# Performance work log

Measured on AMD Instinct MI355X. Metric: run time of the kernel, lower is better.

The kernel has to match this reference:

```python
import jax, jax.numpy as jnp
import numpy as np

N, E, G = 139264, 278528, 8192   # nodes, edges, graphs
H, DIN, DOUT, C = 256, 2, 3, 60
EPS = 1e-5


def setup_inputs() -> dict:
    key = jax.random.key(0)
    ks = jax.random.split(key, 24)
    inp = {
        "node_features": jax.random.normal(ks[0], (N, DIN), jnp.float32),
        "src": jax.random.randint(ks[1], (E,), 0, N, jnp.int32),
        "dst": jax.random.randint(ks[2], (E,), 0, N, jnp.int32),
        "node2graph": jnp.sort(jax.random.randint(ks[3], (N,), 0, G, jnp.int32)),
        "W_emb": jax.random.normal(ks[4], (DIN, H), jnp.float32) * 0.5,
        "b_emb": jnp.zeros((H,), jnp.float32),
        "W_conv1": jax.random.normal(ks[5], (H, H), jnp.float32) / np.sqrt(H),
        "b_conv1": jnp.zeros((H,), jnp.float32),
        "W_conv2": jax.random.normal(ks[6], (H, H), jnp.float32) / np.sqrt(H),
        "b_conv2": jnp.zeros((H,), jnp.float32),
        # 6 BatchNorm layers (2 in block_1, 2 in block_2, 2 in block_3), eval mode
        "bn_gamma": jnp.ones((6, H), jnp.float32),
        "bn_beta": jnp.zeros((6, H), jnp.float32),
        "bn_mean": jax.random.normal(ks[7], (6, H), jnp.float32) * 0.1,
        "bn_var": jax.random.uniform(ks[8], (6, H), jnp.float32, 0.5, 1.5),
        "W_out": jax.random.normal(ks[9], (H, DOUT), jnp.float32) / np.sqrt(H),
        "b_out": jnp.zeros((DOUT,), jnp.float32),
        "W_ci": jax.random.normal(ks[10], (DOUT, H), jnp.float32) * 0.5,
        "b_ci": jnp.zeros((H,), jnp.float32),
        "W_b3a": jax.random.normal(ks[11], (H, H), jnp.float32) / np.sqrt(H),
        "b_b3a": jnp.zeros((H,), jnp.float32),
        "W_b3b": jax.random.normal(ks[12], (H, H), jnp.float32) / np.sqrt(H),
        "b_b3b": jnp.zeros((H,), jnp.float32),
        "W_cls": jax.random.normal(ks[13], (H, C), jnp.float32) / np.sqrt(H),
        "b_cls": jnp.zeros((C,), jnp.float32),
    }
    return inp


def reference(node_features, src, dst, node2graph,
              W_emb, b_emb, W_conv1, b_conv1, W_conv2, b_conv2,
              bn_gamma, bn_beta, bn_mean, bn_var,
              W_out, b_out, W_ci, b_ci,
              W_b3a, b_b3a, W_b3b, b_b3b, W_cls, b_cls):
    ones_e = jnp.ones((E,), jnp.float32)
    deg_out = jnp.clip(jax.ops.segment_sum(ones_e, src, N), 1.0)  # out-degree
    deg_in = jnp.clip(jax.ops.segment_sum(ones_e, dst, N), 1.0)   # in-degree
    n_out = jax.lax.rsqrt(deg_out)[:, None]
    n_in = jax.lax.rsqrt(deg_in)[:, None]

    def graph_conv(x, W, b):  # DGL GraphConv, norm='both'
        m = (x * n_out)[src]                               # [E,H] gather
        agg = jax.ops.segment_sum(m, dst, N)               # [N,H] scatter-add
        return (agg * n_in) @ W + b

    def bn(x, i):  # eval-mode BatchNorm1d
        inv = jax.lax.rsqrt(bn_var[i] + EPS)
        return (x - bn_mean[i]) * (bn_gamma[i] * inv) + bn_beta[i]

    # embedding
    x = node_features @ W_emb + b_emb                      # [N,H]
    # conv block 1 (dropout is identity in eval)
    h = graph_conv(x, W_conv1, b_conv1)
    h = x + jax.nn.relu(bn(jax.nn.relu(bn(h, 0)), 1))
    x = h
    # conv block 2
    h = graph_conv(h, W_conv2, b_conv2)
    h = x + jax.nn.relu(bn(jax.nn.relu(bn(h, 2)), 3))
    # 3D pose head
    h3d = h @ W_out + b_out                                # [N,3]
    # per-graph mean (dgl.mean_nodes)
    gsum = jax.ops.segment_sum(h3d, node2graph, G)         # [G,3]
    gcnt = jnp.clip(jax.ops.segment_sum(jnp.ones((N,), jnp.float32), node2graph, G), 1.0)
    gmean = gsum / gcnt[:, None]
    # classification head
    z = gmean @ W_ci + b_ci
    z = jax.nn.relu(bn(z @ W_b3a + b_b3a, 4))
    z = jax.nn.relu(bn(z @ W_b3b + b_b3b, 5))
    label = z @ W_cls + b_cls                              # [G,60]
    return (h3d, label)
```

## Files before the change

### kernel.cpp

```cpp
#include <hip/hip_runtime.h>


#define NN 139264
#define EE 278528
#define GG 8192
#define NBLK 544
#define EBLK 1088

typedef float f32x4 __attribute__((ext_vector_type(4)));
typedef __bf16 bf16x8 __attribute__((ext_vector_type(8)));
typedef unsigned short u16x8 __attribute__((ext_vector_type(8)));
typedef unsigned short u16x4 __attribute__((ext_vector_type(4)));

__device__ __forceinline__ float bf2f(unsigned short u) {
    unsigned int i = ((unsigned int)u) << 16;
    float f;
    __builtin_memcpy(&f, &i, 4);
    return f;
}
__device__ __forceinline__ unsigned short f2bf(float f) {
    unsigned int i;
    __builtin_memcpy(&i, &f, 4);
    i += 0x7fffu + ((i >> 16) & 1u);
    return (unsigned short)(i >> 16);
}
__device__ __forceinline__ unsigned short bfbits(float f) {
    __bf16 b = (__bf16)f;
    return __builtin_bit_cast(unsigned short, b);
}

#define OFF_DEG_OUT ((size_t)0)
#define OFF_DEG_IN  ((size_t)557056)
#define ZERO_BYTES  ((size_t)1114112)
#define OFF_T       ((size_t)1114112)
#define OFF_NOUT    ((size_t)2785280)
#define OFF_NIN     ((size_t)3342336)
#define OFF_ROWPTR  ((size_t)3899392)
#define OFF_CURSOR  ((size_t)4460544)
#define OFF_CSRS    ((size_t)5017600)
#define OFF_WT2     ((size_t)6131712)
#define OFF_WTA     ((size_t)6262784)
#define OFF_WTB     ((size_t)6393856)
#define OFF_WTCLS   ((size_t)6524928)
#define OFF_WOT     ((size_t)6557696)
#define OFF_BNS     ((size_t)6565888)
#define OFF_BNH     ((size_t)6572032)
#define OFF_TAB     ((size_t)6578176)
#define OFF_PP      ((size_t)6587392)
#define OFF_BSUM    ((size_t)6595584)
#define OFF_R3      ((size_t)6599680)
#define OFF_H1W     ((size_t)8270848)


__global__ void k_deg(const int* __restrict__ src, const int* __restrict__ dst,
                      int* __restrict__ deg_out, int* __restrict__ deg_in) {
    int e = blockIdx.x * 256 + threadIdx.x;
    if (e < EE) {
        atomicAdd(&deg_out[src[e]], 1);
        atomicAdd(&deg_in[dst[e]], 1);
    }
}

__global__ void k_scan1(const int* __restrict__ deg, int* __restrict__ part, int* __restrict__ bsum) {
    __shared__ int sh[256];
    int t = threadIdx.x, gid = blockIdx.x * 256 + t;
    int v = deg[gid];
    sh[t] = v;
    __syncthreads();
#pragma unroll
    for (int off = 1; off < 256; off <<= 1) {
        int a = (t >= off) ? sh[t - off] : 0;
        __syncthreads();
        sh[t] += a;
        __syncthreads();
    }
    part[gid] = sh[t] - v;
    if (t == 255) bsum[blockIdx.x] = sh[t];
}

__global__ void k_scan2(int* __restrict__ bsum) {
    __shared__ int sh[1024];
    int t = threadIdx.x;
    int v = (t < NBLK) ? bsum[t] : 0;
    sh[t] = v;
    __syncthreads();
#pragma unroll
    for (int off = 1; off < 1024; off <<= 1) {
        int a = (t >= off) ? sh[t - off] : 0;
        __syncthreads();
        sh[t] += a;
        __syncthreads();
    }
    if (t < NBLK) bsum[t] = sh[t] - v;
}

__global__ void k_scan3(int* __restrict__ rp, const int* __restrict__ bsum, int* __restrict__ cursor,
                        const int* __restrict__ dego, const int* __restrict__ degi,
                        float* __restrict__ n_out, float* __restrict__ n_in) {
    int t = threadIdx.x, gid = blockIdx.x * 256 + t;
    int v = rp[gid] + bsum[blockIdx.x];
    rp[gid] = v;
    cursor[gid] = v;
    if (gid == 0) rp[NN] = EE;
    n_out[gid] = rsqrtf((float)max(dego[gid], 1));
    n_in[gid]  = rsqrtf((float)max(degi[gid], 1));
}

__global__ void k_fill(const int* __restrict__ src, const int* __restrict__ dst,
                       int* __restrict__ cursor, int* __restrict__ csr) {
    int e = blockIdx.x * 256 + threadIdx.x;
    int d = dst[e];
    int pos = atomicAdd(&cursor[d], 1);
    csr[pos] = src[e];
}

__global__ void k_rowstats(const int* __restrict__ rp, const int* __restrict__ csr,
                           const float* __restrict__ n_out, const float* __restrict__ n_in,
                           const float* __restrict__ nf, float* __restrict__ T) {
    int r = blockIdx.x * 256 + threadIdx.x;
    int e0 = rp[r], e1 = rp[r + 1];
    float S0 = 0.f, S1 = 0.f, S2 = 0.f;
    for (int e = e0; e < e1; e++) {
        int s = csr[e];
        float sc = n_out[s];
        S0 = fmaf(sc, nf[2 * s], S0);
        S1 = fmaf(sc, nf[2 * s + 1], S1);
        S2 += sc;
    }
    float ni = n_in[r];
    T[3 * r]     = S0 * ni;
    T[3 * r + 1] = S1 * ni;
    T[3 * r + 2] = S2 * ni;
}

__global__ void k_prep(const float* __restrict__ Wc2, const float* __restrict__ Wb3a,
                       const float* __restrict__ Wb3b,
                       unsigned short* __restrict__ wt2, unsigned short* __restrict__ wta,
                       unsigned short* __restrict__ wtb,
                       const float* __restrict__ wcls, unsigned short* __restrict__ tcls,
                       const float* __restrict__ g, const float* __restrict__ b,
                       const float* __restrict__ m, const float* __restrict__ v,
                       float* __restrict__ bns, float* __restrict__ bnh,
                       const float* __restrict__ Wout, unsigned short* __restrict__ wot,
                       const float* __restrict__ Wemb, const float* __restrict__ bemb,
                       const float* __restrict__ Wc1, const float* __restrict__ bc1,
                       const float* __restrict__ bc2,
                       float* __restrict__ TAB, float* __restrict__ PP) {
    int t = blockIdx.x * 256 + threadIdx.x;
    int y = blockIdx.y;
    if (y < 3) {
        int k = t >> 8, n = t & 255;
        const float* w = (y == 0) ? Wc2 : (y == 1) ? Wb3a : Wb3b;
        unsigned short* o = (y == 0) ? wt2 : (y == 1) ? wta : wtb;
        o[n * 256 + k] = f2bf(w[t]);
    } else if (y == 3) {
        if (t < 16384) {
            int n = t >> 8, k = t & 255;
            tcls[t] = (n < 60) ? f2bf(wcls[k * 60 + n]) : (unsigned short)0;
        }
    } else if (y == 4) {
        if (t < 1536) {
            float inv = rsqrtf(v[t] + 1e-5f);
            float s = g[t] * inv;
            bns[t] = s;
            bnh[t] = b[t] - m[t] * s;
        }
    } else if (y == 5) {
        if (t < 4096) {
            int n = t >> 8, k = t & 255;
            wot[t] = (n < 3) ? f2bf(Wout[k * 3 + n]) : (unsigned short)0;
        }
    } else if (y == 6) {
        if (t < 256) {
            int c = t;
            float inv0 = rsqrtf(v[c] + 1e-5f);
            float s0 = g[c] * inv0;
            float h0 = b[c] - m[c] * s0;
            float e0 = 0.f, e1 = 0.f, e2 = 0.f;
            for (int k = 0; k < 256; k++) {
                float w = Wc1[k * 256 + c];
                e0 = fmaf(Wemb[k], w, e0);
                e1 = fmaf(Wemb[256 + k], w, e1);
                e2 = fmaf(bemb[k], w, e2);
            }
            TAB[c]        = e0 * s0;
            TAB[256 + c]  = e1 * s0;
            TAB[512 + c]  = e2 * s0;
            TAB[768 + c]  = fmaf(bc1[c], s0, h0);
            float inv1 = rsqrtf(v[256 + c] + 1e-5f);
            float s1 = g[256 + c] * inv1;
            TAB[1024 + c] = s1;
            TAB[1280 + c] = b[256 + c] - m[256 + c] * s1;
            TAB[1536 + c] = Wemb[c];
            TAB[1792 + c] = Wemb[256 + c];
            TAB[2048 + c] = bemb[c];
        }
    } else {
        if (t < 256) {
            int cp = t;
            int w = cp >> 6, rs = (cp >> 2) & 15, nt = cp & 3;
            int c = w * 64 + nt * 16 + rs;
            PP[cp] = bc2[c];
            float inv2 = rsqrtf(v[512 + c] + 1e-5f);
            float s2 = g[512 + c] * inv2;
            PP[256 + cp] = s2;
            PP[512 + cp] = b[512 + c] - m[512 + c] * s2;
            float inv3 = rsqrtf(v[768 + c] + 1e-5f);
            float s3 = g[768 + c] * inv3;
            PP[768 + cp] = s3;
            PP[1024 + cp] = b[768 + c] - m[768 + c] * s3;
            PP[1280 + cp] = Wout[c * 3];
            PP[1536 + cp] = Wout[c * 3 + 1];
            PP[1792 + cp] = Wout[c * 3 + 2];
        }
    }
}

__launch_bounds__(256)
__global__ void k_conv1(const float* __restrict__ T, const float* __restrict__ nf,
                        const float* __restrict__ TAB, const float* __restrict__ n_out,
                        const unsigned short* __restrict__ Wt2, const unsigned short* __restrict__ wot,
                        unsigned short* __restrict__ h1w, float* __restrict__ R3) {
    __shared__ unsigned char tileY[64 * 512];
    int lane = threadIdx.x & 63, wave = threadIdx.x >> 6;
    int wrow = blockIdx.x * 64;
    int rsel = lane & 15, kq = lane >> 4;

    {
        int wu = __builtin_amdgcn_readfirstlane(wave);
        const float* tb = TAB + wu * 64;
        int row = wrow + lane;
        float t0 = T[3 * row], t1 = T[3 * row + 1], t2 = T[3 * row + 2];
        float2 p = *(const float2*)(nf + 2 * (size_t)row);
        float f0 = p.x, f1 = p.y;
        float no = n_out[row];
        int sw = (lane & 7) << 4;
        unsigned char* wb = tileY + lane * 512;
#pragma unroll
        for (int jj = 0; jj < 8; jj++) {
            int co = jj * 8;
            f32x4 ew0a = *(const f32x4*)(tb + co),        ew0b = *(const f32x4*)(tb + co + 4);
            f32x4 ew1a = *(const f32x4*)(tb + 256 + co),  ew1b = *(const f32x4*)(tb + 256 + co + 4);
            f32x4 ew2a = *(const f32x4*)(tb + 512 + co),  ew2b = *(const f32x4*)(tb + 512 + co + 4);
            f32x4 c0a  = *(const f32x4*)(tb + 768 + co),  c0b  = *(const f32x4*)(tb + 768 + co + 4);
            f32x4 s1a  = *(const f32x4*)(tb + 1024 + co), s1b  = *(const f32x4*)(tb + 1024 + co + 4);
            f32x4 h1a  = *(const f32x4*)(tb + 1280 + co), h1b  = *(const f32x4*)(tb + 1280 + co + 4);
            f32x4 w0a  = *(const f32x4*)(tb + 1536 + co), w0b  = *(const f32x4*)(tb + 1536 + co + 4);
            f32x4 w1a  = *(const f32x4*)(tb + 1792 + co), w1b  = *(const f32x4*)(tb + 1792 + co + 4);
            f32x4 bea  = *(const f32x4*)(tb + 2048 + co), beb  = *(const f32x4*)(tb + 2048 + co + 4);
            u16x8 o;
#pragma unroll
            for (int j = 0; j < 4; j++) {
                float z = fmaf(t0, ew0a[j], fmaf(t1, ew1a[j], fmaf(t2, ew2a[j], c0a[j])));
                z = fmaxf(z, 0.f);
                z = fmaxf(fmaf(z, s1a[j], h1a[j]), 0.f);
                float yv = z + fmaf(f0, w0a[j], fmaf(f1, w1a[j], bea[j]));
                o[j] = bfbits(yv * no);
            }
#pragma unroll
            for (int j = 0; j < 4; j++) {
                float z = fmaf(t0, ew0b[j], fmaf(t1, ew1b[j], fmaf(t2, ew2b[j], c0b[j])));
                z = fmaxf(z, 0.f);
                z = fmaxf(fmaf(z, s1b[j], h1b[j]), 0.f);
                float yv = z + fmaf(f0, w0b[j], fmaf(f1, w1b[j], beb[j]));
                o[4 + j] = bfbits(yv * no);
            }
            int cbyte = (wu * 64 + co) * 2;
            *(u16x8*)(wb + (cbyte ^ sw)) = o;
        }
    }
    __syncthreads();

    bool w0w = (wave == 0);
    f32x4 acc[4][4];
    f32x4 acc3[4];
    f32x4 zero = {0.f, 0.f, 0.f, 0.f};
#pragma unroll
    for (int i = 0; i < 4; i++) {
        acc3[i] = zero;
#pragma unroll
        for (int j = 0; j < 4; j++) acc[i][j] = zero;
    }
#pragma unroll
    for (int kt = 0; kt < 8; kt++) {
        int cb = kt * 64 + kq * 16;
        int k0 = kt * 32 + kq * 8;
        bf16x8 afr[4];
#pragma unroll
        for (int mt = 0; mt < 4; mt++) {
            int ar = mt * 16 + rsel;
            u16x8 au = *(const u16x8*)(tileY + ar * 512 + (cb ^ ((ar & 7) << 4)));
            afr[mt] = __builtin_bit_cast(bf16x8, au);
        }
        bf16x8 bfr[4];
#pragma unroll
        for (int nt = 0; nt < 4; nt++) {
            u16x8 bu = *(const u16x8*)(Wt2 + (size_t)(wave * 64 + nt * 16 + rsel) * 256 + k0);
            bfr[nt] = __builtin_bit_cast(bf16x8, bu);
        }
        bf16x8 bw;
        if (w0w) {
            u16x8 bu = *(const u16x8*)(wot + (size_t)rsel * 256 + k0);
            bw = __builtin_bit_cast(bf16x8, bu);
        }
#pragma unroll
        for (int mt = 0; mt < 4; mt++) {
#pragma unroll
            for (int nt = 0; nt < 4; nt++)
                acc[mt][nt] = __builtin_amdgcn_mfma_f32_16x16x32_bf16(afr[mt], bfr[nt], acc[mt][nt], 0, 0, 0);
            if (w0w)
                acc3[mt] = __builtin_amdgcn_mfma_f32_16x16x32_bf16(afr[mt], bw, acc3[mt], 0, 0, 0);
        }
    }

#pragma unroll
    for (int mt = 0; mt < 4; mt++) {
#pragma unroll
        for (int r = 0; r < 4; r++) {
            int row = wrow + mt * 16 + kq * 4 + r;
            u16x4 o;
#pragma unroll
            for (int nt = 0; nt < 4; nt++) o[nt] = bfbits(acc[mt][nt][r]);
            *(u16x4*)(h1w + (size_t)row * 256 + wave * 64 + rsel * 4) = o;
        }
    }

    if (w0w && rsel < 3) {
#pragma unroll
        for (int mt = 0; mt < 4; mt++)
#pragma unroll
            for (int r = 0; r < 4; r++) {
                int row = wrow + mt * 16 + kq * 4 + r;
                R3[(size_t)row * 3 + rsel] = acc3[mt][r] / n_out[row];
            }
    }
}

__launch_bounds__(256)
__global__ void k_gconv(const int* __restrict__ rp, const int* __restrict__ csr,
                        const float* __restrict__ n_in, const unsigned short* __restrict__ h1w,
                        const float* __restrict__ PP, const float* __restrict__ bout,
                        const float* __restrict__ R3, float* __restrict__ h3d) {
    int hw = threadIdx.x >> 5;
    int l = threadIdx.x & 31;
    int c0 = l * 8;

    float bc[8], s0[8], h0[8], s1[8], h1v[8], w0[8], w1[8], w2[8];
#pragma unroll
    for (int j = 0; j < 8; j += 4) {
        *(float4*)(bc + j)  = *(const float4*)(PP + c0 + j);
        *(float4*)(s0 + j)  = *(const float4*)(PP + 256 + c0 + j);
        *(float4*)(h0 + j)  = *(const float4*)(PP + 512 + c0 + j);
        *(float4*)(s1 + j)  = *(const float4*)(PP + 768 + c0 + j);
        *(float4*)(h1v + j) = *(const float4*)(PP + 1024 + c0 + j);
        *(float4*)(w0 + j)  = *(const float4*)(PP + 1280 + c0 + j);
        *(float4*)(w1 + j)  = *(const float4*)(PP + 1536 + c0 + j);
        *(float4*)(w2 + j)  = *(const float4*)(PP + 1792 + c0 + j);
    }
    float b0 = bout[0], b1 = bout[1], b2v = bout[2];

    int rbase = blockIdx.x * 64 + hw * 8;
#pragma unroll 1
    for (int i = 0; i < 8; i++) {
        int row = rbase + i;
        int e0 = rp[row], e1 = rp[row + 1];
        float a[8] = {0.f, 0.f, 0.f, 0.f, 0.f, 0.f, 0.f, 0.f};
        for (int e = e0; e < e1; e++) {
            int s = csr[e];
            u16x8 v = *(const u16x8*)(h1w + ((size_t)s << 8) + c0);
#pragma unroll
            for (int j = 0; j < 8; j++) a[j] += bf2f(v[j]);
        }
        float ni = n_in[row];
        float p0 = 0.f, p1 = 0.f, p2 = 0.f;
#pragma unroll
        for (int j = 0; j < 8; j++) {
            float y = fmaf(a[j], ni, bc[j]);
            y = fmaxf(fmaf(y, s0[j], h0[j]), 0.f);
            y = fmaxf(fmaf(y, s1[j], h1v[j]), 0.f);
            p0 = fmaf(y, w0[j], p0);
            p1 = fmaf(y, w1[j], p1);
            p2 = fmaf(y, w2[j], p2);
        }
#pragma unroll
        for (int m = 1; m < 32; m <<= 1) {
            p0 += __shfl_xor(p0, m, 32);
            p1 += __shfl_xor(p1, m, 32);
            p2 += __shfl_xor(p2, m, 32);
        }
        if (l == 0) {
            size_t o = (size_t)row * 3;
            h3d[o]     = p0 + R3[o]     + b0;
            h3d[o + 1] = p1 + R3[o + 1] + b1;
            h3d[o + 2] = p2 + R3[o + 2] + b2v;
        }
    }
}

__launch_bounds__(64)
__global__ void k_head(const int* __restrict__ n2g, const float* __restrict__ h3d,
                       const float* __restrict__ Wci, const float* __restrict__ bci,
                       const unsigned short* __restrict__ wta, const float* __restrict__ ba,
                       const unsigned short* __restrict__ wtb, const float* __restrict__ bb,
                       const unsigned short* __restrict__ wtcls, const float* __restrict__ bcls,
                       const float* __restrict__ bns, const float* __restrict__ bnh,
                       float* __restrict__ label) {
    __shared__ unsigned char tileA[8192];
    __shared__ unsigned char tileB[8192];
    int lane = threadIdx.x;
    int wrow = blockIdx.x * 16;
    int rsel = lane & 15, kq = lane >> 4;
    int g = wrow + rsel;

    int lo = 0, hi = NN;
    while (lo < hi) { int mid = (lo + hi) >> 1; if (n2g[mid] < g) lo = mid + 1; else hi = mid; }
    int s = lo;
    hi = NN;
    while (lo < hi) { int mid = (lo + hi) >> 1; if (n2g[mid] < g + 1) lo = mid + 1; else hi = mid; }
    int e = lo;
    float m0 = 0.f, m1 = 0.f, m2 = 0.f;
    for (int j = s; j < e; j++) {
        m0 += h3d[(size_t)j * 3];
        m1 += h3d[(size_t)j * 3 + 1];
        m2 += h3d[(size_t)j * 3 + 2];
    }
    float inv = 1.f / fmaxf((float)(e - s), 1.f);
    m0 *= inv; m1 *= inv; m2 *= inv;

    f32x4 zero = {0.f, 0.f, 0.f, 0.f};
    f32x4 acc[16];
#pragma unroll
    for (int i = 0; i < 16; i++) acc[i] = zero;

#pragma unroll
    for (int kt = 0; kt < 8; kt++) {
        int k0 = kt * 32 + kq * 8;
        u16x8 au;
#pragma unroll
        for (int j = 0; j < 8; j++)
            au[j] = f2bf(fmaf(m0, Wci[k0 + j], fmaf(m1, Wci[256 + k0 + j],
                         fmaf(m2, Wci[512 + k0 + j], bci[k0 + j]))));
        bf16x8 af = __builtin_bit_cast(bf16x8, au);
#pragma unroll
        for (int nt = 0; nt < 16; nt++) {
            u16x8 bu = *(const u16x8*)(wta + (size_t)(nt * 16 + rsel) * 256 + k0);
            acc[nt] = __builtin_amdgcn_mfma_f32_16x16x32_bf16(af, __builtin_bit_cast(bf16x8, bu), acc[nt], 0, 0, 0);
        }
    }
#pragma unroll
    for (int nt = 0; nt < 16; nt++) {
        int col = nt * 16 + rsel;
        float bcv = ba[col];
        float sc = bns[4 * 256 + col], h = bnh[4 * 256 + col];
#pragma unroll
        for (int r = 0; r < 4; r++) {
            float y = fmaxf(fmaf(acc[nt][r] + bcv, sc, h), 0.f);
            int rr = kq * 4 + r;
            *(unsigned short*)(tileA + rr * 512 + ((col * 2) ^ ((rr & 7) << 4))) = f2bf(y);
        }
    }

#pragma unroll
    for (int i = 0; i < 16; i++) acc[i] = zero;
#pragma unroll
    for (int kt = 0; kt < 8; kt++) {
        int cb = kt * 64 + kq * 16;
        u16x8 au = *(const u16x8*)(tileA + rsel * 512 + (cb ^ ((rsel & 7) << 4)));
        bf16x8 af = __builtin_bit_cast(bf16x8, au);
        int k0 = kt * 32 + kq * 8;
#pragma unroll
        for (int nt = 0; nt < 16; nt++) {
            u16x8 bu = *(const u16x8*)(wtb + (size_t)(nt * 16 + rsel) * 256 + k0);
            acc[nt] = __builtin_amdgcn_mfma_f32_16x16x32_bf16(af, __builtin_bit_cast(bf16x8, bu), acc[nt], 0, 0, 0);
        }
    }
#pragma unroll
    for (int nt = 0; nt < 16; nt++) {
        int col = nt * 16 + rsel;
        float bcv = bb[col];
        float sc = bns[5 * 256 + col], h = bnh[5 * 256 + col];
#pragma unroll
        for (int r = 0; r < 4; r++) {
            float y = fmaxf(fmaf(acc[nt][r] + bcv, sc, h), 0.f);
            int rr = kq * 4 + r;
            *(unsigned short*)(tileB + rr * 512 + ((col * 2) ^ ((rr & 7) << 4))) = f2bf(y);
        }
    }

    f32x4 acc3[4];
#pragma unroll
    for (int i = 0; i < 4; i++) acc3[i] = zero;
#pragma unroll
    for (int kt = 0; kt < 8; kt++) {
        int cb = kt * 64 + kq * 16;
        u16x8 au = *(const u16x8*)(tileB + rsel * 512 + (cb ^ ((rsel & 7) << 4)));
        bf16x8 af = __builtin_bit_cast(bf16x8, au);
        int k0 = kt * 32 + kq * 8;
#pragma unroll
        for (int nt = 0; nt < 4; nt++) {
            u16x8 bu = *(const u16x8*)(wtcls + (size_t)(nt * 16 + rsel) * 256 + k0);
            acc3[nt] = __builtin_amdgcn_mfma_f32_16x16x32_bf16(af, __builtin_bit_cast(bf16x8, bu), acc3[nt], 0, 0, 0);
        }
    }
    int rowb = wrow + kq * 4;
#pragma unroll
    for (int nt = 0; nt < 4; nt++) {
        int col = nt * 16 + rsel;
        if (col < 60) {
            float bcv = bcls[col];
#pragma unroll
            for (int r = 0; r < 4; r++)
                label[(size_t)(rowb + r) * 60 + col] = acc3[nt][r] + bcv;
        }
    }
}

extern "C" void kernel_launch(void* const* d_in, const int* in_sizes, int n_in,
                              void* d_out, int out_size, void* d_ws, size_t ws_size,
                              hipStream_t stream) {
    const float* nf   = (const float*)d_in[0];
    const int* src    = (const int*)d_in[1];
    const int* dst    = (const int*)d_in[2];
    const int* n2g    = (const int*)d_in[3];
    const float* Wemb = (const float*)d_in[4];
    const float* bemb = (const float*)d_in[5];
    const float* Wc1  = (const float*)d_in[6];
    const float* bc1  = (const float*)d_in[7];
    const float* Wc2  = (const float*)d_in[8];
    const float* bc2  = (const float*)d_in[9];
    const float* bng  = (const float*)d_in[10];
    const float* bnb  = (const float*)d_in[11];
    const float* bnm  = (const float*)d_in[12];
    const float* bnv  = (const float*)d_in[13];
    const float* Wout = (const float*)d_in[14];
    const float* bout = (const float*)d_in[15];
    const float* Wci  = (const float*)d_in[16];
    const float* bci  = (const float*)d_in[17];
    const float* Wb3a = (const float*)d_in[18];
    const float* bb3a = (const float*)d_in[19];
    const float* Wb3b = (const float*)d_in[20];
    const float* bb3b = (const float*)d_in[21];
    const float* Wcls = (const float*)d_in[22];
    const float* bcls = (const float*)d_in[23];

    char* ws = (char*)d_ws;
    int* deg_out = (int*)(ws + OFF_DEG_OUT);
    int* deg_in  = (int*)(ws + OFF_DEG_IN);
    float* T     = (float*)(ws + OFF_T);
    float* n_out = (float*)(ws + OFF_NOUT);
    float* n_inp = (float*)(ws + OFF_NIN);
    int* row_ptr = (int*)(ws + OFF_ROWPTR);
    int* cursor  = (int*)(ws + OFF_CURSOR);
    int* csr_src = (int*)(ws + OFF_CSRS);
    int* bsum    = (int*)(ws + OFF_BSUM);
    unsigned short* wt2   = (unsigned short*)(ws + OFF_WT2);
    unsigned short* wta   = (unsigned short*)(ws + OFF_WTA);
    unsigned short* wtb   = (unsigned short*)(ws + OFF_WTB);
    unsigned short* wtcls = (unsigned short*)(ws + OFF_WTCLS);
    unsigned short* wot   = (unsigned short*)(ws + OFF_WOT);
    float* bns = (float*)(ws + OFF_BNS);
    float* bnh = (float*)(ws + OFF_BNH);
    float* TAB = (float*)(ws + OFF_TAB);
    float* PP  = (float*)(ws + OFF_PP);
    float* R3  = (float*)(ws + OFF_R3);
    unsigned short* h1w = (unsigned short*)(ws + OFF_H1W);

    float* h3d_out   = (float*)d_out;
    float* label_out = (float*)d_out + (size_t)NN * 3;

    hipMemsetAsync(ws, 0, ZERO_BYTES, stream);

    k_deg<<<EBLK, 256, 0, stream>>>(src, dst, deg_out, deg_in);
    k_scan1<<<NBLK, 256, 0, stream>>>(deg_in, row_ptr, bsum);
    k_scan2<<<1, 1024, 0, stream>>>(bsum);
    k_scan3<<<NBLK, 256, 0, stream>>>(row_ptr, bsum, cursor, deg_out, deg_in, n_out, n_inp);
    k_fill<<<EBLK, 256, 0, stream>>>(src, dst, cursor, csr_src);
    k_prep<<<dim3(256, 8), 256, 0, stream>>>(Wc2, Wb3a, Wb3b, wt2, wta, wtb,
                                             Wcls, wtcls, bng, bnb, bnm, bnv, bns, bnh,
                                             Wout, wot, Wemb, bemb, Wc1, bc1, bc2, TAB, PP);
    k_rowstats<<<NBLK, 256, 0, stream>>>(row_ptr, csr_src, n_out, n_inp, nf, T);

    k_conv1<<<NN / 64, 256, 0, stream>>>(T, nf, TAB, n_out, wt2, wot, h1w, R3);
    k_gconv<<<NN / 64, 256, 0, stream>>>(row_ptr, csr_src, n_inp, h1w, PP, bout, R3, h3d_out);
    k_head<<<GG / 16, 64, 0, stream>>>(n2g, h3d_out, Wci, bci, wta, bb3a, wtb, bb3b,
                                       wtcls, bcls, bns, bnh, label_out);
}
```

Baseline: 230.1 us.

## Merge graph preprocessing kernels into one cooperative kernel with grid syncs

Replaces the memset plus seven preprocessing launches (degree count, three-stage scan, CSR fill, weight prep, row stats) with a single cooperative kernel that separates the phases with grid.sync(). The block-sum scan now runs in one block using three elements per thread. The goal is to remove launch gaps and per-kernel ramp-up between these small stages. In exchange it adds several grid-wide barriers, and it needs all 544 blocks to be co-resident; if they are not, the cooperative launch can fail.

```diff
diff --git a/kernel.cpp b/kernel.cpp
--- a/kernel.cpp
+++ b/kernel.cpp
@@ -1,11 +1,13 @@
 #include <hip/hip_runtime.h>
-
+#include <hip/hip_cooperative_groups.h>
+
+
+namespace cg = cooperative_groups;
 
 #define NN 139264
 #define EE 278528
 #define GG 8192
 #define NBLK 544
-#define EBLK 1088
 
 typedef float f32x4 __attribute__((ext_vector_type(4)));
 typedef __bf16 bf16x8 __attribute__((ext_vector_type(8)));
@@ -31,7 +33,6 @@
 
 #define OFF_DEG_OUT ((size_t)0)
 #define OFF_DEG_IN  ((size_t)557056)
-#define ZERO_BYTES  ((size_t)1114112)
 #define OFF_T       ((size_t)1114112)
 #define OFF_NOUT    ((size_t)2785280)
 #define OFF_NIN     ((size_t)3342336)
@@ -51,168 +52,176 @@
 #define OFF_R3      ((size_t)6599680)
 #define OFF_H1W     ((size_t)8270848)
 
-
-__global__ void k_deg(const int* __restrict__ src, const int* __restrict__ dst,
-                      int* __restrict__ deg_out, int* __restrict__ deg_in) {
-    int e = blockIdx.x * 256 + threadIdx.x;
-    if (e < EE) {
+__launch_bounds__(256)
+__global__ void k_gprep(const int* __restrict__ src, const int* __restrict__ dst,
+                        const float* __restrict__ nf,
+                        int* __restrict__ deg_out, int* __restrict__ deg_in,
+                        int* __restrict__ rp, int* __restrict__ cursor, int* __restrict__ csr,
+                        float* __restrict__ n_out, float* __restrict__ n_in,
+                        int* __restrict__ bsum, float* __restrict__ T,
+                        const float* __restrict__ Wc2, const float* __restrict__ Wb3a,
+                        const float* __restrict__ Wb3b,
+                        unsigned short* __restrict__ wt2, unsigned short* __restrict__ wta,
+                        unsigned short* __restrict__ wtb,
+                        const float* __restrict__ wcls, unsigned short* __restrict__ tcls,
+                        const float* __restrict__ bng, const float* __restrict__ bnb,
+                        const float* __restrict__ bnm, const float* __restrict__ bnv,
+                        float* __restrict__ bns, float* __restrict__ bnh,
+                        const float* __restrict__ Wout, unsigned short* __restrict__ wot,
+                        const float* __restrict__ Wemb, const float* __restrict__ bemb,
+                        const float* __restrict__ Wc1, const float* __restrict__ bc1,
+                        const float* __restrict__ bc2,
+                        float* __restrict__ TAB, float* __restrict__ PP) {
+    cg::grid_group grid = cg::this_grid();
+    __shared__ int sh[256];
+    __shared__ int shS[NBLK];
+    __shared__ int shT[256];
+    int tid = threadIdx.x;
+    int gtid = blockIdx.x * 256 + tid;
+
+    deg_out[gtid] = 0;
+    deg_in[gtid] = 0;
+    if (gtid < 65536) {
+        int k = gtid >> 8, n = gtid & 255;
+        wt2[n * 256 + k] = f2bf(Wc2[gtid]);
+        wta[n * 256 + k] = f2bf(Wb3a[gtid]);
+        wtb[n * 256 + k] = f2bf(Wb3b[gtid]);
+    }
+    if (gtid < 16384) {
+        int n = gtid >> 8, k = gtid & 255;
+        tcls[gtid] = (n < 60) ? f2bf(wcls[k * 60 + n]) : (unsigned short)0;
+    }
+    if (gtid < 1536) {
+        float inv = rsqrtf(bnv[gtid] + 1e-5f);
+        float s = bng[gtid] * inv;
+        bns[gtid] = s;
+        bnh[gtid] = bnb[gtid] - bnm[gtid] * s;
+    }
+    if (gtid < 4096) {
+        int n = gtid >> 8, k = gtid & 255;
+        wot[gtid] = (n < 3) ? f2bf(Wout[k * 3 + n]) : (unsigned short)0;
+    }
+    if (gtid >= 131072 && gtid < 131328) {
+        int c = gtid - 131072;
+        float inv0 = rsqrtf(bnv[c] + 1e-5f);
+        float s0 = bng[c] * inv0;
+        float h0 = bnb[c] - bnm[c] * s0;
+        float e0 = 0.f, e1 = 0.f, e2 = 0.f;
+        for (int k = 0; k < 256; k++) {
+            float w = Wc1[k * 256 + c];
+            e0 = fmaf(Wemb[k], w, e0);
+            e1 = fmaf(Wemb[256 + k], w, e1);
+            e2 = fmaf(bemb[k], w, e2);
+        }
+        TAB[c]        = e0 * s0;
+        TAB[256 + c]  = e1 * s0;
+        TAB[512 + c]  = e2 * s0;
+        TAB[768 + c]  = fmaf(bc1[c], s0, h0);
+        float inv1 = rsqrtf(bnv[256 + c] + 1e-5f);
+        float s1 = bng[256 + c] * inv1;
+        TAB[1024 + c] = s1;
+        TAB[1280 + c] = bnb[256 + c] - bnm[256 + c] * s1;
+        TAB[1536 + c] = Wemb[c];
+        TAB[1792 + c] = Wemb[256 + c];
+        TAB[2048 + c] = bemb[c];
+    }
+    if (gtid >= 131328 && gtid < 131584) {
+        int cp = gtid - 131328;
+        int w = cp >> 6, rs = (cp >> 2) & 15, nt = cp & 3;
+        int c = w * 64 + nt * 16 + rs;
+        PP[cp] = bc2[c];
+        float inv2 = rsqrtf(bnv[512 + c] + 1e-5f);
+        float s2 = bng[512 + c] * inv2;
+        PP[256 + cp] = s2;
+        PP[512 + cp] = bnb[512 + c] - bnm[512 + c] * s2;
+        float inv3 = rsqrtf(bnv[768 + c] + 1e-5f);
+        float s3 = bng[768 + c] * inv3;
+        PP[768 + cp] = s3;
+        PP[1024 + cp] = bnb[768 + c] - bnm[768 + c] * s3;
+        PP[1280 + cp] = Wout[c * 3];
+        PP[1536 + cp] = Wout[c * 3 + 1];
+        PP[1792 + cp] = Wout[c * 3 + 2];
+    }
+    grid.sync();
+
+    for (int e = gtid; e < EE; e += NN) {
         atomicAdd(&deg_out[src[e]], 1);
         atomicAdd(&deg_in[dst[e]], 1);
     }
-}
-
-__global__ void k_scan1(const int* __restrict__ deg, int* __restrict__ part, int* __restrict__ bsum) {
-    __shared__ int sh[256];
-    int t = threadIdx.x, gid = blockIdx.x * 256 + t;
-    int v = deg[gid];
-    sh[t] = v;
-    __syncthreads();
-#pragma unroll
-    for (int off = 1; off < 256; off <<= 1) {
-        int a = (t >= off) ? sh[t - off] : 0;
+    grid.sync();
+
+    {
+        int v = deg_in[gtid];
+        sh[tid] = v;
         __syncthreads();
-        sh[t] += a;
+#pragma unroll
+        for (int off = 1; off < 256; off <<= 1) {
+            int a = (tid >= off) ? sh[tid - off] : 0;
+            __syncthreads();
+            sh[tid] += a;
+            __syncthreads();
+        }
+        rp[gtid] = sh[tid] - v;
+        if (tid == 255) bsum[blockIdx.x] = sh[tid];
+    }
+    grid.sync();
+
+    if (blockIdx.x == 0) {
+        for (int i = tid; i < NBLK; i += 256) shS[i] = bsum[i];
         __syncthreads();
-    }
-    part[gid] = sh[t] - v;
-    if (t == 255) bsum[blockIdx.x] = sh[t];
-}
-
-__global__ void k_scan2(int* __restrict__ bsum) {
-    __shared__ int sh[1024];
-    int t = threadIdx.x;
-    int v = (t < NBLK) ? bsum[t] : 0;
-    sh[t] = v;
-    __syncthreads();
-#pragma unroll
-    for (int off = 1; off < 1024; off <<= 1) {
-        int a = (t >= off) ? sh[t - off] : 0;
+        int i0 = 3 * tid;
+        int a0 = (i0 < NBLK) ? shS[i0] : 0;
+        int a1 = (i0 + 1 < NBLK) ? shS[i0 + 1] : 0;
+        int a2 = (i0 + 2 < NBLK) ? shS[i0 + 2] : 0;
+        int S = a0 + a1 + a2;
+        shT[tid] = S;
         __syncthreads();
-        sh[t] += a;
-        __syncthreads();
-    }
-    if (t < NBLK) bsum[t] = sh[t] - v;
-}
-
-__global__ void k_scan3(int* __restrict__ rp, const int* __restrict__ bsum, int* __restrict__ cursor,
-                        const int* __restrict__ dego, const int* __restrict__ degi,
-                        float* __restrict__ n_out, float* __restrict__ n_in) {
-    int t = threadIdx.x, gid = blockIdx.x * 256 + t;
-    int v = rp[gid] + bsum[blockIdx.x];
-    rp[gid] = v;
-    cursor[gid] = v;
-    if (gid == 0) rp[NN] = EE;
-    n_out[gid] = rsqrtf((float)max(dego[gid], 1));
-    n_in[gid]  = rsqrtf((float)max(degi[gid], 1));
-}
-
-__global__ void k_fill(const int* __restrict__ src, const int* __restrict__ dst,
-                       int* __restrict__ cursor, int* __restrict__ csr) {
-    int e = blockIdx.x * 256 + threadIdx.x;
-    int d = dst[e];
-    int pos = atomicAdd(&cursor[d], 1);
-    csr[pos] = src[e];
-}
-
-__global__ void k_rowstats(const int* __restrict__ rp, const int* __restrict__ csr,
-                           const float* __restrict__ n_out, const float* __restrict__ n_in,
-                           const float* __restrict__ nf, float* __restrict__ T) {
-    int r = blockIdx.x * 256 + threadIdx.x;
-    int e0 = rp[r], e1 = rp[r + 1];
-    float S0 = 0.f, S1 = 0.f, S2 = 0.f;
-    for (int e = e0; e < e1; e++) {
-        int s = csr[e];
-        float sc = n_out[s];
-        S0 = fmaf(sc, nf[2 * s], S0);
-        S1 = fmaf(sc, nf[2 * s + 1], S1);
-        S2 += sc;
-    }
-    float ni = n_in[r];
-    T[3 * r]     = S0 * ni;
-    T[3 * r + 1] = S1 * ni;
-    T[3 * r + 2] = S2 * ni;
-}
-
-__global__ void k_prep(const float* __restrict__ Wc2, const float* __restrict__ Wb3a,
-                       const float* __restrict__ Wb3b,
-                       unsigned short* __restrict__ wt2, unsigned short* __restrict__ wta,
-                       unsigned short* __restrict__ wtb,
-                       const float* __restrict__ wcls, unsigned short* __restrict__ tcls,
-                       const float* __restrict__ g, const float* __restrict__ b,
-                       const float* __restrict__ m, const float* __restrict__ v,
-                       float* __restrict__ bns, float* __restrict__ bnh,
-                       const float* __restrict__ Wout, unsigned short* __restrict__ wot,
-                       const float* __restrict__ Wemb, const float* __restrict__ bemb,
-                       const float* __restrict__ Wc1, const float* __restrict__ bc1,
-                       const float* __restrict__ bc2,
-                       float* __restrict__ TAB, float* __restrict__ PP) {
-    int t = blockIdx.x * 256 + threadIdx.x;
-    int y = blockIdx.y;
-    if (y < 3) {
-        int k = t >> 8, n = t & 255;
-        const float* w = (y == 0) ? Wc2 : (y == 1) ? Wb3a : Wb3b;
-        unsigned short* o = (y == 0) ? wt2 : (y == 1) ? wta : wtb;
-        o[n * 256 + k] = f2bf(w[t]);
-    } else if (y == 3) {
-        if (t < 16384) {
-            int n = t >> 8, k = t & 255;
-            tcls[t] = (n < 60) ? f2bf(wcls[k * 60 + n]) : (unsigned short)0;
-        }
-    } else if (y == 4) {
-        if (t < 1536) {
-            float inv = rsqrtf(v[t] + 1e-5f);
-            float s = g[t] * inv;
-            bns[t] = s;
-            bnh[t] = b[t] - m[t] * s;
-        }
-    } else if (y == 5) {
-        if (t < 4096) {
-            int n = t >> 8, k = t & 255;
-            wot[t] = (n < 3) ? f2bf(Wout[k * 3 + n]) : (unsigned short)0;
-        }
-    } else if (y == 6) {
-        if (t < 256) {
-            int c = t;
-            float inv0 = rsqrtf(v[c] + 1e-5f);
-            float s0 = g[c] * inv0;
-            float h0 = b[c] - m[c] * s0;
-            float e0 = 0.f, e1 = 0.f, e2 = 0.f;
-            for (int k = 0; k < 256; k++) {
-                float w = Wc1[k * 256 + c];
-                e0 = fmaf(Wemb[k], w, e0);
-                e1 = fmaf(Wemb[256 + k], w, e1);
-                e2 = fmaf(bemb[k], w, e2);
-            }
-            TAB[c]        = e0 * s0;
-            TAB[256 + c]  = e1 * s0;
-            TAB[512 + c]  = e2 * s0;
-            TAB[768 + c]  = fmaf(bc1[c], s0, h0);
-            float inv1 = rsqrtf(v[256 + c] + 1e-5f);
-            float s1 = g[256 + c] * inv1;
-            TAB[1024 + c] = s1;
-            TAB[1280 + c] = b[256 + c] - m[256 + c] * s1;
-            TAB[1536 + c] = Wemb[c];
-            TAB[1792 + c] = Wemb[256 + c];
-            TAB[2048 + c] = bemb[c];
-        }
-    } else {
-        if (t < 256) {
-            int cp = t;
-            int w = cp >> 6, rs = (cp >> 2) & 15, nt = cp & 3;
-            int c = w * 64 + nt * 16 + rs;
-            PP[cp] = bc2[c];
-            float inv2 = rsqrtf(v[512 + c] + 1e-5f);
-            float s2 = g[512 + c] * inv2;
-            PP[256 + cp] = s2;
-            PP[512 + cp] = b[512 + c] - m[512 + c] * s2;
-            float inv3 = rsqrtf(v[768 + c] + 1e-5f);
-            float s3 = g[768 + c] * inv3;
-            PP[768 + cp] = s3;
-            PP[1024 + cp] = b[768 + c] - m[768 + c] * s3;
-            PP[1280 + cp] = Wout[c * 3];
-            PP[1536 + cp] = Wout[c * 3 + 1];
-            PP[1792 + cp] = Wout[c * 3 + 2];
-        }
+#pragma unroll
+        for (int off = 1; off < 256; off <<= 1) {
+            int a = (tid >= off) ? shT[tid - off] : 0;
+            __syncthreads();
+            shT[tid] += a;
+            __syncthreads();
+        }
+        int P = shT[tid] - S;
+        if (i0 < NBLK)     bsum[i0]     = P;
+        if (i0 + 1 < NBLK) bsum[i0 + 1] = P + a0;
+        if (i0 + 2 < NBLK) bsum[i0 + 2] = P + a0 + a1;
+    }
+    grid.sync();
+
+    {
+        int v = rp[gtid] + bsum[blockIdx.x];
+        rp[gtid] = v;
+        cursor[gtid] = v;
+        if (gtid == 0) rp[NN] = EE;
+        n_out[gtid] = rsqrtf((float)max(deg_out[gtid], 1));
+        n_in[gtid]  = rsqrtf((float)max(deg_in[gtid], 1));
+    }
+    grid.sync();
+
+    for (int e = gtid; e < EE; e += NN) {
+        int d = dst[e];
+        int pos = atomicAdd(&cursor[d], 1);
+        csr[pos] = src[e];
+    }
+    grid.sync();
+
+    {
+        int r = gtid;
+        int e0 = rp[r], e1 = rp[r + 1];
+        float S0 = 0.f, S1 = 0.f, S2 = 0.f;
+        for (int e = e0; e < e1; e++) {
+            int s = csr[e];
+            float sc = n_out[s];
+            S0 = fmaf(sc, nf[2 * s], S0);
+            S1 = fmaf(sc, nf[2 * s + 1], S1);
+            S2 += sc;
+        }
+        float ni = n_in[r];
+        T[3 * r]     = S0 * ni;
+        T[3 * r + 1] = S1 * ni;
+        T[3 * r + 2] = S2 * ni;
     }
 }
 
@@ -568,17 +577,21 @@
     float* h3d_out   = (float*)d_out;
     float* label_out = (float*)d_out + (size_t)NN * 3;
 
-    hipMemsetAsync(ws, 0, ZERO_BYTES, stream);
-
-    k_deg<<<EBLK, 256, 0, stream>>>(src, dst, deg_out, deg_in);
-    k_scan1<<<NBLK, 256, 0, stream>>>(deg_in, row_ptr, bsum);
-    k_scan2<<<1, 1024, 0, stream>>>(bsum);
-    k_scan3<<<NBLK, 256, 0, stream>>>(row_ptr, bsum, cursor, deg_out, deg_in, n_out, n_inp);
-    k_fill<<<EBLK, 256, 0, stream>>>(src, dst, cursor, csr_src);
-    k_prep<<<dim3(256, 8), 256, 0, stream>>>(Wc2, Wb3a, Wb3b, wt2, wta, wtb,
-                                             Wcls, wtcls, bng, bnb, bnm, bnv, bns, bnh,
-                                             Wout, wot, Wemb, bemb, Wc1, bc1, bc2, TAB, PP);
-    k_rowstats<<<NBLK, 256, 0, stream>>>(row_ptr, csr_src, n_out, n_inp, nf, T);
+    void* args[] = {
+        (void*)&src, (void*)&dst, (void*)&nf,
+        (void*)&deg_out, (void*)&deg_in, (void*)&row_ptr, (void*)&cursor, (void*)&csr_src,
+        (void*)&n_out, (void*)&n_inp, (void*)&bsum, (void*)&T,
+        (void*)&Wc2, (void*)&Wb3a, (void*)&Wb3b,
+        (void*)&wt2, (void*)&wta, (void*)&wtb,
+        (void*)&Wcls, (void*)&wtcls,
+        (void*)&bng, (void*)&bnb, (void*)&bnm, (void*)&bnv,
+        (void*)&bns, (void*)&bnh,
+        (void*)&Wout, (void*)&wot,
+        (void*)&Wemb, (void*)&bemb,
+        (void*)&Wc1, (void*)&bc1, (void*)&bc2,
+        (void*)&TAB, (void*)&PP
+    };
+    hipLaunchCooperativeKernel((const void*)k_gprep, dim3(NBLK), dim3(256), args, 0, stream);
 
     k_conv1<<<NN / 64, 256, 0, stream>>>(T, nf, TAB, n_out, wt2, wot, h1w, R3);
     k_gconv<<<NN / 64, 256, 0, stream>>>(row_ptr, csr_src, n_inp, h1w, PP, bout, R3, h3d_out);
```

Result: slower. 587.6 us (+155.4%).
